# Kernel optimization log

Measured on AMD Instinct MI355X. Metric: run time of the kernel, lower is better.

The kernel has to match this reference:

```python
import jax, jax.numpy as jnp
import numpy as np

H = 8        # num_heads
DH = 64      # head_dim
DV = 64      # value_dim
DQ = 256     # query_dim
DHIT = 256   # hit_feature_dim
DMLP = 512   # query_dim * mlp_hidden_dim_multiplier
EPS = 1e-5


def _layernorm(x, g, b):
    m = jnp.mean(x, axis=-1, keepdims=True)
    v = jnp.mean(jnp.square(x - m), axis=-1, keepdims=True)
    return (x - m) * jax.lax.rsqrt(v + EPS) * g + b


def setup_inputs() -> dict:
    key = jax.random.key(0)
    ks = jax.random.split(key, 10)
    B, K, N = 8, 64, 16384
    s = 0.02
    return {
        "slot_representations": jax.random.normal(ks[0], (B, K, DQ), jnp.float32),
        "hit_features": jax.random.normal(ks[1], (B, N, DHIT), jnp.float32),
        "ln1_g": jnp.ones((DQ,), jnp.float32),
        "ln1_b": jnp.zeros((DQ,), jnp.float32),
        "Wq": jax.random.normal(ks[2], (DQ, H * DH), jnp.float32) * s,
        "Wk": jax.random.normal(ks[3], (DHIT, H * DH), jnp.float32) * s,
        "Wv": jax.random.normal(ks[4], (DHIT, H * DV), jnp.float32) * s,
        "W1": jax.random.normal(ks[5], (H * DV, DMLP), jnp.float32) * s,
        "b1": jnp.zeros((DMLP,), jnp.float32),
        "W2": jax.random.normal(ks[6], (DMLP, DQ), jnp.float32) * s,
        "b2": jnp.zeros((DQ,), jnp.float32),
        "ln2_g": jnp.ones((DQ,), jnp.float32),
        "ln2_b": jnp.zeros((DQ,), jnp.float32),
    }


def reference(slot_representations, hit_features, ln1_g, ln1_b, Wq, Wk, Wv,
              W1, b1, W2, b2, ln2_g, ln2_b):
    B, K, _ = slot_representations.shape
    _, N, _ = hit_features.shape
    scale = DH ** -0.5
    slots_norm = _layernorm(slot_representations, ln1_g, ln1_b)
    q = (slots_norm @ Wq).reshape(B, K, H, DH)          # [B,K,H,DH]
    k = (hit_features @ Wk).reshape(B, N, H, DH)        # [B,N,H,DH]
    v = (hit_features @ Wv).reshape(B, N, H, DV)        # [B,N,H,DV]
    logits = jnp.einsum('bkhd,bnhd->bhkn', q, k) * scale
    attn = jax.nn.softmax(logits, axis=-1)              # [B,H,K,N]
    att_v = jnp.einsum('bhkn,bnhd->bkhd', attn, v).reshape(B, K, H * DV)
    mlp_out = jax.nn.relu(att_v @ W1 + b1) @ W2 + b2
    return _layernorm(slot_representations + mlp_out, ln2_g, ln2_b)
```

## Files before the change

kernel.cpp:

```cpp
#include <hip/hip_runtime.h>
#include <hip/hip_bf16.h>

#define HH   8
#define Bb   8
#define Kk   64
#define Nn   16384
#define DQd  256
#define EPSf 1e-5f
#define NCH  32
#define CHK  512
#define SUB  32
#define NSUB (CHK / SUB)

typedef __bf16 bf16_t;
typedef __bf16 bf16x8 __attribute__((ext_vector_type(8)));
typedef __bf16 bf16x4 __attribute__((ext_vector_type(4)));
typedef __bf16 bf16x2 __attribute__((ext_vector_type(2)));
typedef float  f32x4  __attribute__((ext_vector_type(4)));
typedef float  f32x16 __attribute__((ext_vector_type(16)));

#define MFMA16(a, b, c) __builtin_amdgcn_mfma_f32_16x16x32_bf16((a), (b), (c), 0, 0, 0)
#define MFMA32(a, b, c) __builtin_amdgcn_mfma_f32_32x32x16_bf16((a), (b), (c), 0, 0, 0)

static __device__ __forceinline__ int pk2(float x, float y) {
    bf16x2 v; v[0] = (bf16_t)x; v[1] = (bf16_t)y;
    return __builtin_bit_cast(int, v);
}

static __device__ __forceinline__ void pack_tile(const f32x16 Sv, int hi, bf16x8* out) {
    #pragma unroll
    for (int kc = 0; kc < 2; ++kc) {
        const int oc = kc * 8;
        int Lp0 = pk2(Sv[oc + 0], Sv[oc + 1]);
        int Lp1 = pk2(Sv[oc + 2], Sv[oc + 3]);
        int Hp0 = pk2(Sv[oc + 4], Sv[oc + 5]);
        int Hp1 = pk2(Sv[oc + 6], Sv[oc + 7]);
        int Lx0 = __shfl_xor(Lp0, 32, 64);
        int Lx1 = __shfl_xor(Lp1, 32, 64);
        int Hx0 = __shfl_xor(Hp0, 32, 64);
        int Hx1 = __shfl_xor(Hp1, 32, 64);
        int4 bi;
        bi.x = hi ? Hx0 : Lp0;
        bi.y = hi ? Hx1 : Lp1;
        bi.z = hi ? Hp0 : Lx0;
        bi.w = hi ? Hp1 : Lx1;
        out[kc] = __builtin_bit_cast(bf16x8, bi);
    }
}

static __device__ __forceinline__ void store8(bf16_t* dst, float4 a, float4 b) {
    bf16x8 o;
    o[0] = (bf16_t)a.x; o[1] = (bf16_t)a.y; o[2] = (bf16_t)a.z; o[3] = (bf16_t)a.w;
    o[4] = (bf16_t)b.x; o[5] = (bf16_t)b.y; o[6] = (bf16_t)b.z; o[7] = (bf16_t)b.w;
    *(bf16x8*)dst = o;
}

__global__ __launch_bounds__(256) void k0_ln(
    const float* __restrict__ slots, const float* __restrict__ g1,
    const float* __restrict__ bb1, const float* __restrict__ Wv,
    bf16_t* __restrict__ norm, bf16_t* __restrict__ WvT)
{
    const int t = threadIdx.x;
    if (blockIdx.x >= 32) {
        const int h = blockIdx.x - 32;
        const int dv = t & 63, dq = t >> 6;
        #pragma unroll
        for (int i = 0; i < 16; ++i) {
            int d = dq * 64 + i * 4;
            bf16x4 o;
            #pragma unroll
            for (int j = 0; j < 4; ++j)
                o[j] = (bf16_t)Wv[(size_t)(d + j) * 512 + h * 64 + dv];
            *(bf16x4*)&WvT[(size_t)(h * 64 + dv) * 256 + d] = o;
        }
        return;
    }
    const int b = blockIdx.x >> 2, rg = blockIdx.x & 3;
    const int w = t >> 6, lane = t & 63;
    float4 gv = *(const float4*)&g1[lane * 4];
    float4 bv = *(const float4*)&bb1[lane * 4];
    #pragma unroll
    for (int i = 0; i < 4; ++i) {
        int row = rg * 16 + w * 4 + i;
        float4 x = *(const float4*)&slots[((size_t)b * Kk + row) * DQd + lane * 4];
        float s = x.x + x.y + x.z + x.w;
        for (int m = 1; m < 64; m <<= 1) s += __shfl_xor(s, m, 64);
        float mean = s * (1.0f / 256.0f);
        float dx = x.x - mean, dy = x.y - mean, dz = x.z - mean, dw = x.w - mean;
        float v2 = dx * dx + dy * dy + dz * dz + dw * dw;
        for (int m = 1; m < 64; m <<= 1) v2 += __shfl_xor(v2, m, 64);
        float rs = rsqrtf(v2 * (1.0f / 256.0f) + EPSf);
        bf16x4 o;
        o[0] = (bf16_t)(dx * rs * gv.x + bv.x);
        o[1] = (bf16_t)(dy * rs * gv.y + bv.y);
        o[2] = (bf16_t)(dz * rs * gv.z + bv.z);
        o[3] = (bf16_t)(dw * rs * gv.w + bv.w);
        *(bf16x4*)&norm[((size_t)b * Kk + row) * 256 + lane * 4] = o;
    }
}

__global__ __launch_bounds__(256) void k0m(
    const float* __restrict__ Wq, const float* __restrict__ Wk,
    bf16_t* __restrict__ MT)
{
    __shared__ float scr4[4][32 * 33];
    const int h = blockIdx.x >> 2, rt = blockIdx.x & 3;
    const int t = threadIdx.x;
    const int w = t >> 6, lane = t & 63, l31 = lane & 31, hi = lane >> 5;

    f32x16 acc[2][2] = {};
    for (int kc = 0; kc < 4; ++kc) {
        bf16x8 af[2], bfr[2];
        #pragma unroll
        for (int mt = 0; mt < 2; ++mt) {
            const float* src = &Wq[(size_t)(w * 64 + mt * 32 + l31) * 512 + h * 64 + kc * 16 + hi * 8];
            float4 u0 = ((const float4*)src)[0], u1 = ((const float4*)src)[1];
            af[mt][0] = (bf16_t)u0.x; af[mt][1] = (bf16_t)u0.y;
            af[mt][2] = (bf16_t)u0.z; af[mt][3] = (bf16_t)u0.w;
            af[mt][4] = (bf16_t)u1.x; af[mt][5] = (bf16_t)u1.y;
            af[mt][6] = (bf16_t)u1.z; af[mt][7] = (bf16_t)u1.w;
        }
        #pragma unroll
        for (int nt = 0; nt < 2; ++nt) {
            const float* src = &Wk[(size_t)(rt * 64 + nt * 32 + l31) * 512 + h * 64 + kc * 16 + hi * 8];
            float4 u0 = ((const float4*)src)[0], u1 = ((const float4*)src)[1];
            bfr[nt][0] = (bf16_t)u0.x; bfr[nt][1] = (bf16_t)u0.y;
            bfr[nt][2] = (bf16_t)u0.z; bfr[nt][3] = (bf16_t)u0.w;
            bfr[nt][4] = (bf16_t)u1.x; bfr[nt][5] = (bf16_t)u1.y;
            bfr[nt][6] = (bf16_t)u1.z; bfr[nt][7] = (bf16_t)u1.w;
        }
        #pragma unroll
        for (int mt = 0; mt < 2; ++mt)
            #pragma unroll
            for (int nt = 0; nt < 2; ++nt)
                acc[mt][nt] = MFMA32(af[mt], bfr[nt], acc[mt][nt]);
    }
    float* scr = scr4[w];
    #pragma unroll
    for (int mt = 0; mt < 2; ++mt)
        for (int nt = 0; nt < 2; ++nt) {
            #pragma unroll
            for (int r = 0; r < 16; ++r) {
                int m = (r & 3) + 8 * (r >> 2) + 4 * hi;
                scr[m * 33 + l31] = acc[mt][nt][r] * 0.125f;
            }
            #pragma unroll
            for (int j = 0; j < 16; ++j) {
                int c = rt * 64 + nt * 32 + hi * 16 + j;
                MT[((size_t)(h * 256 + c)) * 256 + w * 64 + mt * 32 + l31]
                    = (bf16_t)scr[l31 * 33 + hi * 16 + j];
            }
        }
}

__global__ __launch_bounds__(256) void k1n(
    const bf16_t* __restrict__ norm, const bf16_t* __restrict__ MT,
    bf16_t* __restrict__ qt)
{
    __shared__ float scr4[4][32 * 33];
    const int bid = blockIdx.x;
    const int ch = bid & 1, h = (bid >> 1) & 7, b = bid >> 4;
    const int t = threadIdx.x;
    const int w = t >> 6, lane = t & 63, l31 = lane & 31, hi = lane >> 5;
    const int colbase = ch * 128 + w * 32;

    const bf16_t* mbase = MT + ((size_t)(h * 256 + colbase + l31)) * 256 + hi * 8;
    const bf16_t* nbase = norm + ((size_t)(b * 64 + l31)) * 256 + hi * 8;

    f32x16 acc[2] = {};
    for (int kc = 0; kc < 16; ++kc) {
        bf16x8 af = *(const bf16x8*)(mbase + kc * 16);
        bf16x8 b0 = *(const bf16x8*)(nbase + kc * 16);
        bf16x8 b1 = *(const bf16x8*)(nbase + (size_t)32 * 256 + kc * 16);
        acc[0] = MFMA32(af, b0, acc[0]);
        acc[1] = MFMA32(af, b1, acc[1]);
    }
    float* scr = scr4[w];
    size_t qbase = (size_t)(b * HH + h) * 64;
    #pragma unroll
    for (int nt = 0; nt < 2; ++nt) {
        #pragma unroll
        for (int r = 0; r < 16; ++r) {
            int m = (r & 3) + 8 * (r >> 2) + 4 * hi;
            scr[m * 33 + l31] = acc[nt][r];
        }
        #pragma unroll
        for (int j = 0; j < 16; ++j) {
            qt[(qbase + nt * 32 + hi * 16 + j) * 256 + colbase + l31]
                = (bf16_t)scr[l31 * 33 + hi * 16 + j];
        }
    }
}

__global__ __launch_bounds__(512) void k3_attn(
    const float* __restrict__ hit, const bf16_t* __restrict__ qt,
    const bf16_t* __restrict__ WvT, bf16_t* __restrict__ nump,
    float* __restrict__ lp)
{
    __shared__ alignas(16) bf16_t hs[2][SUB * 256];
    __shared__ alignas(16) bf16_t vb[2][16 * 512];

    const int bid = blockIdx.x;
    const int c  = bid & 31;
    const int hg = (bid >> 5) & 1;
    const int b  = bid >> 6;
    const int t  = threadIdx.x;
    const int w = t >> 6, lane = t & 63;
    const int l31 = lane & 31, hi = lane >> 5;
    const int hl = w >> 1;
    const int qh = w & 1;
    const int h  = hg * 4 + hl;
    const int bh = b * HH + h;

    bf16x8 qf[16], wf[16];
    {
        const bf16_t* qrow = qt + ((size_t)bh * 64 + qh * 32 + l31) * 256 + hi * 8;
        const bf16_t* wrow = WvT + ((size_t)(h * 64 + qh * 32 + l31)) * 256 + hi * 8;
        #pragma unroll
        for (int ks = 0; ks < 16; ++ks) {
            qf[ks] = *(const bf16x8*)(qrow + ks * 16);
            wf[ks] = *(const bf16x8*)(wrow + ks * 16);
        }
    }

    f32x16 accO = {};
    f32x16 accX = {};
    float ls = 0.f;

    const float* hbase = hit + ((size_t)b * Nn + c * CHK) * 256;
    const int row0 = t >> 5, g0 = t & 31;
    const int sw0 = (g0 ^ (row0 & 7)) * 8;
    const int sw1 = (g0 ^ ((row0 + 16) & 7)) * 8;

    float4 pA0, pA1, pB0, pB1;
#define PREFETCH(ss) do { \
        const float* s0_ = hbase + (size_t)(ss) * SUB * 256 + (size_t)row0 * 256 + g0 * 8; \
        pA0 = ((const float4*)s0_)[0]; pA1 = ((const float4*)s0_)[1]; \
        const float* s1_ = s0_ + 16 * 256; \
        pB0 = ((const float4*)s1_)[0]; pB1 = ((const float4*)s1_)[1]; \
    } while (0)

    PREFETCH(0);
    store8(&hs[0][row0 * 256 + sw0], pA0, pA1);
    store8(&hs[0][(row0 + 16) * 256 + sw1], pB0, pB1);
    PREFETCH(1);
    __syncthreads();

    const int xr = l31 & 7;

    for (int s = 0; s < NSUB; ++s) {
        const int cur = s & 1;
        const bf16_t* hrow = &hs[cur][l31 * 256];

        f32x16 St = {}, Vt = {};
        #pragma unroll
        for (int ks = 0; ks < 16; ++ks) {
            bf16x8 A = *(const bf16x8*)(hrow + (((2 * ks + hi) ^ xr) * 8));
            Vt = MFMA32(A, wf[ks], Vt);
            St = MFMA32(A, qf[ks], St);
        }

        if (s + 1 < NSUB) {
            store8(&hs[cur ^ 1][row0 * 256 + sw0], pA0, pA1);
            store8(&hs[cur ^ 1][(row0 + 16) * 256 + sw1], pB0, pB1);
        }
        if (s + 2 < NSUB) PREFETCH(s + 2);

        #pragma unroll
        for (int r = 0; r < 16; ++r) {
            float e = __expf(St[r]);
            St[r] = e;
            ls += e;
        }
        bf16x8 Pf[2];
        pack_tile(St, hi, Pf);
        {
            bf16x8 Vf[2];
            pack_tile(Vt, hi, Vf);
            *(bf16x8*)&vb[cur][((hl * 2 + 0) * 2 + qh) * 512 + lane * 8] = Vf[0];
            *(bf16x8*)&vb[cur][((hl * 2 + 1) * 2 + qh) * 512 + lane * 8] = Vf[1];
        }
        __syncthreads();

        {
            bf16x8 vo0 = *(const bf16x8*)&vb[cur][((hl * 2 + 0) * 2 + qh) * 512 + lane * 8];
            bf16x8 vx0 = *(const bf16x8*)&vb[cur][((hl * 2 + 0) * 2 + (1 - qh)) * 512 + lane * 8];
            bf16x8 vo1 = *(const bf16x8*)&vb[cur][((hl * 2 + 1) * 2 + qh) * 512 + lane * 8];
            bf16x8 vx1 = *(const bf16x8*)&vb[cur][((hl * 2 + 1) * 2 + (1 - qh)) * 512 + lane * 8];
            accO = MFMA32(Pf[0], vo0, accO);
            accX = MFMA32(Pf[0], vx0, accX);
            accO = MFMA32(Pf[1], vo1, accO);
            accX = MFMA32(Pf[1], vx1, accX);
        }
    }
#undef PREFETCH

    {
        float lt = ls + __shfl_xor(ls, 32, 64);
        if (hi == 0)
            lp[((size_t)bh * NCH + c) * 64 + qh * 32 + l31] = lt;
    }
    {
        size_t nbase = ((size_t)bh * NCH + c) * 64 * 64;
        #pragma unroll
        for (int r = 0; r < 16; ++r) {
            int q = qh * 32 + (r & 3) + 8 * (r >> 2) + 4 * hi;
            size_t ro = nbase + (size_t)q * 64;
            nump[ro + qh * 32 + l31]       = (bf16_t)accO[r];
            nump[ro + (1 - qh) * 32 + l31] = (bf16_t)accX[r];
        }
    }
}

__global__ __launch_bounds__(256) void k35_comb(
    const bf16_t* __restrict__ nump, const float* __restrict__ lp,
    bf16_t* __restrict__ X)
{
    const int bh = blockIdx.x >> 1, qhb = blockIdx.x & 1;
    const int b = bh >> 3, h = bh & 7;
    const int t = threadIdx.x;
    const int q = qhb * 32 + (t >> 3), g = t & 7;
    float s8[8] = {};
    float lsum = 0.f;
    #pragma unroll 4
    for (int cc = 0; cc < NCH; ++cc) {
        size_t base = ((size_t)bh * NCH + cc) * 64 + q;
        bf16x8 v = *(const bf16x8*)&nump[base * 64 + g * 8];
        #pragma unroll
        for (int j = 0; j < 8; ++j) s8[j] += (float)v[j];
        lsum += lp[base];
    }
    float inv = 1.0f / lsum;
    bf16x8 o;
    #pragma unroll
    for (int j = 0; j < 8; ++j) o[j] = (bf16_t)(s8[j] * inv);
    *(bf16x8*)&X[((size_t)b * 64 + q) * 512 + h * 64 + g * 8] = o;
}

__global__ __launch_bounds__(256) void k4a_mlp1(
    const bf16_t* __restrict__ X, const float* __restrict__ W1,
    const float* __restrict__ b1, bf16_t* __restrict__ H)
{
    __shared__ float scr[32 * 33];
    const int rt = blockIdx.x >> 4, ct = blockIdx.x & 15;
    const int t = threadIdx.x;
    const int w = t >> 6, lane = t & 63, l31 = lane & 31, hi = lane >> 5;
    const int colbase = ct * 32;

    for (int i = t; i < 32 * 33; i += 256) scr[i] = 0.f;

    const bf16_t* xrow = X + ((size_t)(rt * 32 + l31)) * 512 + hi * 8;
    f32x16 acc = {};
    #pragma unroll
    for (int k8 = 0; k8 < 8; ++k8) {
        int kc = w * 8 + k8;
        bf16x8 af;
        #pragma unroll
        for (int j = 0; j < 8; ++j)
            af[j] = (bf16_t)W1[(size_t)(kc * 16 + hi * 8 + j) * 512 + colbase + l31];
        bf16x8 bfr = *(const bf16x8*)(xrow + kc * 16);
        acc = MFMA32(af, bfr, acc);
    }
    __syncthreads();
    #pragma unroll
    for (int r = 0; r < 16; ++r) {
        int m = (r & 3) + 8 * (r >> 2) + 4 * hi;
        atomicAdd(&scr[m * 33 + l31], acc[r]);
    }
    __syncthreads();
    const float bia = b1[colbase + l31];
    #pragma unroll
    for (int jj = 0; jj < 4; ++jj) {
        int j = w * 4 + jj;
        float v = scr[l31 * 33 + hi * 16 + j] + bia;
        v = fmaxf(v, 0.f);
        H[((size_t)(rt * 32 + hi * 16 + j)) * 512 + colbase + l31] = (bf16_t)v;
    }
}

__global__ __launch_bounds__(256) void k4b_gemm(
    const bf16_t* __restrict__ H, const float* __restrict__ W2,
    const float* __restrict__ b2, const float* __restrict__ slots,
    float* __restrict__ ys)
{
    __shared__ float scr[32 * 33];
    const int b = blockIdx.x >> 4, rtt = (blockIdx.x >> 3) & 1, ct = blockIdx.x & 7;
    const int t = threadIdx.x;
    const int w = t >> 6, lane = t & 63, l31 = lane & 31, hi = lane >> 5;
    const int colbase = ct * 32;
    const int rowbase = b * 64 + rtt * 32;

    for (int i = t; i < 32 * 33; i += 256) scr[i] = 0.f;

    const bf16_t* hrow = H + ((size_t)(rowbase + l31)) * 512 + hi * 8;
    f32x16 acc = {};
    #pragma unroll
    for (int k8 = 0; k8 < 8; ++k8) {
        int kc = w * 8 + k8;
        bf16x8 af;
        #pragma unroll
        for (int j = 0; j < 8; ++j)
            af[j] = (bf16_t)W2[(size_t)(kc * 16 + hi * 8 + j) * 256 + colbase + l31];
        bf16x8 bfr = *(const bf16x8*)(hrow + kc * 16);
        acc = MFMA32(af, bfr, acc);
    }
    __syncthreads();
    #pragma unroll
    for (int r = 0; r < 16; ++r) {
        int m = (r & 3) + 8 * (r >> 2) + 4 * hi;
        atomicAdd(&scr[m * 33 + l31], acc[r]);
    }
    __syncthreads();
    const float b2c = b2[colbase + l31];
    #pragma unroll
    for (int jj = 0; jj < 4; ++jj) {
        int j = w * 4 + jj;
        int row = rowbase + hi * 16 + j;
        float v = scr[l31 * 33 + hi * 16 + j] + b2c
                + slots[(size_t)row * 256 + colbase + l31];
        ys[(size_t)row * 256 + colbase + l31] = v;
    }
}

__global__ __launch_bounds__(256) void k4c_ln2(
    const float* __restrict__ ys, const float* __restrict__ g2,
    const float* __restrict__ bb2, float* __restrict__ out)
{
    const int t = threadIdx.x;
    const int w = t >> 6, lane = t & 63;
    float4 gv = *(const float4*)&g2[lane * 4];
    float4 bv = *(const float4*)&bb2[lane * 4];
    #pragma unroll
    for (int rr = 0; rr < 2; ++rr) {
        int row = blockIdx.x * 8 + w * 2 + rr;
        float4 x = *(const float4*)&ys[(size_t)row * 256 + lane * 4];
        float s = x.x + x.y + x.z + x.w;
        for (int m = 1; m < 64; m <<= 1) s += __shfl_xor(s, m, 64);
        float mean = s * (1.0f / 256.0f);
        float dx = x.x - mean, dy = x.y - mean, dz = x.z - mean, dw = x.w - mean;
        float v2 = dx * dx + dy * dy + dz * dz + dw * dw;
        for (int m = 1; m < 64; m <<= 1) v2 += __shfl_xor(v2, m, 64);
        float rs = rsqrtf(v2 * (1.0f / 256.0f) + EPSf);
        float4 o;
        o.x = dx * rs * gv.x + bv.x;
        o.y = dy * rs * gv.y + bv.y;
        o.z = dz * rs * gv.z + bv.z;
        o.w = dw * rs * gv.w + bv.w;
        *(float4*)&out[(size_t)row * 256 + lane * 4] = o;
    }
}

extern "C" void kernel_launch(void* const* d_in, const int* in_sizes, int n_in,
                              void* d_out, int out_size, void* d_ws, size_t ws_size,
                              hipStream_t stream) {
    (void)in_sizes; (void)n_in; (void)out_size; (void)ws_size;
    const float* slots = (const float*)d_in[0];
    const float* hit   = (const float*)d_in[1];
    const float* g1    = (const float*)d_in[2];
    const float* bb1   = (const float*)d_in[3];
    const float* Wq    = (const float*)d_in[4];
    const float* Wk    = (const float*)d_in[5];
    const float* Wv    = (const float*)d_in[6];
    const float* W1    = (const float*)d_in[7];
    const float* b1v   = (const float*)d_in[8];
    const float* W2    = (const float*)d_in[9];
    const float* b2v   = (const float*)d_in[10];
    const float* g2    = (const float*)d_in[11];
    const float* bb2   = (const float*)d_in[12];
    float* out = (float*)d_out;

    char* wsp = (char*)d_ws;
    bf16_t* qt   = (bf16_t*)wsp;
    float*  ys   = (float*) wsp;
    bf16_t* WvT  = (bf16_t*)(wsp + (size_t)2097152);
    bf16_t* nump = (bf16_t*)(wsp + (size_t)2359296);
    bf16_t* MT   = (bf16_t*)(wsp + (size_t)2359296);
    bf16_t* norm = (bf16_t*)(wsp + (size_t)2359296 + 1048576);
    float*  lp   = (float*) (wsp + (size_t)19136512);
    bf16_t* X    = (bf16_t*)(wsp + (size_t)19660800);
    bf16_t* H    = (bf16_t*)(wsp + (size_t)20185088);

    hipLaunchKernelGGL(k0_ln, dim3(40), dim3(256), 0, stream,
                       slots, g1, bb1, Wv, norm, WvT);
    hipLaunchKernelGGL(k0m, dim3(32), dim3(256), 0, stream,
                       Wq, Wk, MT);
    hipLaunchKernelGGL(k1n, dim3(128), dim3(256), 0, stream,
                       norm, MT, qt);
    hipLaunchKernelGGL(k3_attn, dim3(Bb * 2 * NCH), dim3(512), 0, stream,
                       hit, qt, WvT, nump, lp);
    hipLaunchKernelGGL(k35_comb, dim3(128), dim3(256), 0, stream,
                       nump, lp, X);
    hipLaunchKernelGGL(k4a_mlp1, dim3(256), dim3(256), 0, stream,
                       X, W1, b1v, H);
    hipLaunchKernelGGL(k4b_gemm, dim3(128), dim3(256), 0, stream,
                       H, W2, b2v, slots, ys);
    hipLaunchKernelGGL(k4c_ln2, dim3(64), dim3(256), 0, stream,
                       ys, g2, bb2, out);
}
```

Measured before the change: 295.5 us.

## Fuse weight-prep kernels and merge final GEMM with residual LayerNorm

Merges the two prologue kernels (LayerNorm/Wv transpose and the Wq·Wk^T product) into one launch by block-index dispatch. Fuses the W2 GEMM, bias, residual add and final LayerNorm into a single kernel that keeps the pre-norm rows in shared memory instead of writing them to workspace. This removes two kernel launches and a global round trip for the intermediate, but the fused tail runs on only 16 blocks, each doing a full K=512 reduction serially per wave with uncoalesced W2 loads. That shrinks parallelism in the tail considerably.

```diff
diff --git a/kernel.cpp b/kernel.cpp
--- a/kernel.cpp
+++ b/kernel.cpp
@@ -55,12 +55,65 @@
     *(bf16x8*)dst = o;
 }
 
-__global__ __launch_bounds__(256) void k0_ln(
+__global__ __launch_bounds__(256) void k0_all(
     const float* __restrict__ slots, const float* __restrict__ g1,
-    const float* __restrict__ bb1, const float* __restrict__ Wv,
-    bf16_t* __restrict__ norm, bf16_t* __restrict__ WvT)
+    const float* __restrict__ bb1, const float* __restrict__ Wq,
+    const float* __restrict__ Wk, const float* __restrict__ Wv,
+    bf16_t* __restrict__ norm, bf16_t* __restrict__ WvT,
+    bf16_t* __restrict__ MT)
 {
     const int t = threadIdx.x;
+    if (blockIdx.x >= 40) {
+        __shared__ float scr4[4][32 * 33];
+        const int idm = blockIdx.x - 40;
+        const int h = idm >> 2, rt = idm & 3;
+        const int w = t >> 6, lane = t & 63, l31 = lane & 31, hi = lane >> 5;
+
+        f32x16 acc[2][2] = {};
+        for (int kc = 0; kc < 4; ++kc) {
+            bf16x8 af[2], bfr[2];
+            #pragma unroll
+            for (int mt = 0; mt < 2; ++mt) {
+                const float* src = &Wq[(size_t)(w * 64 + mt * 32 + l31) * 512 + h * 64 + kc * 16 + hi * 8];
+                float4 u0 = ((const float4*)src)[0], u1 = ((const float4*)src)[1];
+                af[mt][0] = (bf16_t)u0.x; af[mt][1] = (bf16_t)u0.y;
+                af[mt][2] = (bf16_t)u0.z; af[mt][3] = (bf16_t)u0.w;
+                af[mt][4] = (bf16_t)u1.x; af[mt][5] = (bf16_t)u1.y;
+                af[mt][6] = (bf16_t)u1.z; af[mt][7] = (bf16_t)u1.w;
+            }
+            #pragma unroll
+            for (int nt = 0; nt < 2; ++nt) {
+                const float* src = &Wk[(size_t)(rt * 64 + nt * 32 + l31) * 512 + h * 64 + kc * 16 + hi * 8];
+                float4 u0 = ((const float4*)src)[0], u1 = ((const float4*)src)[1];
+                bfr[nt][0] = (bf16_t)u0.x; bfr[nt][1] = (bf16_t)u0.y;
+                bfr[nt][2] = (bf16_t)u0.z; bfr[nt][3] = (bf16_t)u0.w;
+                bfr[nt][4] = (bf16_t)u1.x; bfr[nt][5] = (bf16_t)u1.y;
+                bfr[nt][6] = (bf16_t)u1.z; bfr[nt][7] = (bf16_t)u1.w;
+            }
+            #pragma unroll
+            for (int mt = 0; mt < 2; ++mt)
+                #pragma unroll
+                for (int nt = 0; nt < 2; ++nt)
+                    acc[mt][nt] = MFMA32(af[mt], bfr[nt], acc[mt][nt]);
+        }
+        float* scr = scr4[w];
+        #pragma unroll
+        for (int mt = 0; mt < 2; ++mt)
+            for (int nt = 0; nt < 2; ++nt) {
+                #pragma unroll
+                for (int r = 0; r < 16; ++r) {
+                    int m = (r & 3) + 8 * (r >> 2) + 4 * hi;
+                    scr[m * 33 + l31] = acc[mt][nt][r] * 0.125f;
+                }
+                #pragma unroll
+                for (int j = 0; j < 16; ++j) {
+                    int c = rt * 64 + nt * 32 + hi * 16 + j;
+                    MT[((size_t)(h * 256 + c)) * 256 + w * 64 + mt * 32 + l31]
+                        = (bf16_t)scr[l31 * 33 + hi * 16 + j];
+                }
+            }
+        return;
+    }
     if (blockIdx.x >= 32) {
         const int h = blockIdx.x - 32;
         const int dv = t & 63, dq = t >> 6;
@@ -99,60 +152,6 @@
     }
 }
 
-__global__ __launch_bounds__(256) void k0m(
-    const float* __restrict__ Wq, const float* __restrict__ Wk,
-    bf16_t* __restrict__ MT)
-{
-    __shared__ float scr4[4][32 * 33];
-    const int h = blockIdx.x >> 2, rt = blockIdx.x & 3;
-    const int t = threadIdx.x;
-    const int w = t >> 6, lane = t & 63, l31 = lane & 31, hi = lane >> 5;
-
-    f32x16 acc[2][2] = {};
-    for (int kc = 0; kc < 4; ++kc) {
-        bf16x8 af[2], bfr[2];
-        #pragma unroll
-        for (int mt = 0; mt < 2; ++mt) {
-            const float* src = &Wq[(size_t)(w * 64 + mt * 32 + l31) * 512 + h * 64 + kc * 16 + hi * 8];
-            float4 u0 = ((const float4*)src)[0], u1 = ((const float4*)src)[1];
-            af[mt][0] = (bf16_t)u0.x; af[mt][1] = (bf16_t)u0.y;
-            af[mt][2] = (bf16_t)u0.z; af[mt][3] = (bf16_t)u0.w;
-            af[mt][4] = (bf16_t)u1.x; af[mt][5] = (bf16_t)u1.y;
-            af[mt][6] = (bf16_t)u1.z; af[mt][7] = (bf16_t)u1.w;
-        }
-        #pragma unroll
-        for (int nt = 0; nt < 2; ++nt) {
-            const float* src = &Wk[(size_t)(rt * 64 + nt * 32 + l31) * 512 + h * 64 + kc * 16 + hi * 8];
-            float4 u0 = ((const float4*)src)[0], u1 = ((const float4*)src)[1];
-            bfr[nt][0] = (bf16_t)u0.x; bfr[nt][1] = (bf16_t)u0.y;
-            bfr[nt][2] = (bf16_t)u0.z; bfr[nt][3] = (bf16_t)u0.w;
-            bfr[nt][4] = (bf16_t)u1.x; bfr[nt][5] = (bf16_t)u1.y;
-            bfr[nt][6] = (bf16_t)u1.z; bfr[nt][7] = (bf16_t)u1.w;
-        }
-        #pragma unroll
-        for (int mt = 0; mt < 2; ++mt)
-            #pragma unroll
-            for (int nt = 0; nt < 2; ++nt)
-                acc[mt][nt] = MFMA32(af[mt], bfr[nt], acc[mt][nt]);
-    }
-    float* scr = scr4[w];
-    #pragma unroll
-    for (int mt = 0; mt < 2; ++mt)
-        for (int nt = 0; nt < 2; ++nt) {
-            #pragma unroll
-            for (int r = 0; r < 16; ++r) {
-                int m = (r & 3) + 8 * (r >> 2) + 4 * hi;
-                scr[m * 33 + l31] = acc[mt][nt][r] * 0.125f;
-            }
-            #pragma unroll
-            for (int j = 0; j < 16; ++j) {
-                int c = rt * 64 + nt * 32 + hi * 16 + j;
-                MT[((size_t)(h * 256 + c)) * 256 + w * 64 + mt * 32 + l31]
-                    = (bf16_t)scr[l31 * 33 + hi * 16 + j];
-            }
-        }
-}
-
 __global__ __launch_bounds__(256) void k1n(
     const bf16_t* __restrict__ norm, const bf16_t* __restrict__ MT,
     bf16_t* __restrict__ qt)
@@ -378,75 +377,70 @@
     }
 }
 
-__global__ __launch_bounds__(256) void k4b_gemm(
+__global__ __launch_bounds__(256) void k4bc(
     const bf16_t* __restrict__ H, const float* __restrict__ W2,
     const float* __restrict__ b2, const float* __restrict__ slots,
-    float* __restrict__ ys)
-{
-    __shared__ float scr[32 * 33];
-    const int b = blockIdx.x >> 4, rtt = (blockIdx.x >> 3) & 1, ct = blockIdx.x & 7;
+    const float* __restrict__ g2, const float* __restrict__ bb2,
+    float* __restrict__ out)
+{
+    __shared__ float ysL[32 * 260];
+    __shared__ float scr4[4][32 * 33];
+    const int b = blockIdx.x >> 1, rhalf = blockIdx.x & 1;
+    const int rowbase = b * 64 + rhalf * 32;
     const int t = threadIdx.x;
     const int w = t >> 6, lane = t & 63, l31 = lane & 31, hi = lane >> 5;
-    const int colbase = ct * 32;
-    const int rowbase = b * 64 + rtt * 32;
-
-    for (int i = t; i < 32 * 33; i += 256) scr[i] = 0.f;
 
     const bf16_t* hrow = H + ((size_t)(rowbase + l31)) * 512 + hi * 8;
-    f32x16 acc = {};
-    #pragma unroll
-    for (int k8 = 0; k8 < 8; ++k8) {
-        int kc = w * 8 + k8;
-        bf16x8 af;
-        #pragma unroll
-        for (int j = 0; j < 8; ++j)
-            af[j] = (bf16_t)W2[(size_t)(kc * 16 + hi * 8 + j) * 256 + colbase + l31];
-        bf16x8 bfr = *(const bf16x8*)(hrow + kc * 16);
-        acc = MFMA32(af, bfr, acc);
+    float* scr = scr4[w];
+
+    #pragma unroll
+    for (int mc = 0; mc < 2; ++mc) {
+        const int colbase = w * 64 + mc * 32;
+        f32x16 acc = {};
+        for (int kc = 0; kc < 32; ++kc) {
+            bf16x8 af;
+            #pragma unroll
+            for (int j = 0; j < 8; ++j)
+                af[j] = (bf16_t)W2[(size_t)(kc * 16 + hi * 8 + j) * 256 + colbase + l31];
+            bf16x8 bfr = *(const bf16x8*)(hrow + kc * 16);
+            acc = MFMA32(af, bfr, acc);
+        }
+        const float b2c = b2[colbase + l31];
+        #pragma unroll
+        for (int r = 0; r < 16; ++r) {
+            int m = (r & 3) + 8 * (r >> 2) + 4 * hi;
+            scr[m * 33 + l31] = acc[r];
+        }
+        #pragma unroll
+        for (int j = 0; j < 16; ++j) {
+            int rl = hi * 16 + j;
+            float v = scr[l31 * 33 + rl] + b2c
+                    + slots[(size_t)(rowbase + rl) * 256 + colbase + l31];
+            ysL[rl * 260 + colbase + l31] = v;
+        }
     }
     __syncthreads();
-    #pragma unroll
-    for (int r = 0; r < 16; ++r) {
-        int m = (r & 3) + 8 * (r >> 2) + 4 * hi;
-        atomicAdd(&scr[m * 33 + l31], acc[r]);
-    }
-    __syncthreads();
-    const float b2c = b2[colbase + l31];
-    #pragma unroll
-    for (int jj = 0; jj < 4; ++jj) {
-        int j = w * 4 + jj;
-        int row = rowbase + hi * 16 + j;
-        float v = scr[l31 * 33 + hi * 16 + j] + b2c
-                + slots[(size_t)row * 256 + colbase + l31];
-        ys[(size_t)row * 256 + colbase + l31] = v;
-    }
-}
-
-__global__ __launch_bounds__(256) void k4c_ln2(
-    const float* __restrict__ ys, const float* __restrict__ g2,
-    const float* __restrict__ bb2, float* __restrict__ out)
-{
-    const int t = threadIdx.x;
-    const int w = t >> 6, lane = t & 63;
-    float4 gv = *(const float4*)&g2[lane * 4];
-    float4 bv = *(const float4*)&bb2[lane * 4];
-    #pragma unroll
-    for (int rr = 0; rr < 2; ++rr) {
-        int row = blockIdx.x * 8 + w * 2 + rr;
-        float4 x = *(const float4*)&ys[(size_t)row * 256 + lane * 4];
-        float s = x.x + x.y + x.z + x.w;
-        for (int m = 1; m < 64; m <<= 1) s += __shfl_xor(s, m, 64);
-        float mean = s * (1.0f / 256.0f);
-        float dx = x.x - mean, dy = x.y - mean, dz = x.z - mean, dw = x.w - mean;
-        float v2 = dx * dx + dy * dy + dz * dz + dw * dw;
-        for (int m = 1; m < 64; m <<= 1) v2 += __shfl_xor(v2, m, 64);
-        float rs = rsqrtf(v2 * (1.0f / 256.0f) + EPSf);
-        float4 o;
-        o.x = dx * rs * gv.x + bv.x;
-        o.y = dy * rs * gv.y + bv.y;
-        o.z = dz * rs * gv.z + bv.z;
-        o.w = dw * rs * gv.w + bv.w;
-        *(float4*)&out[(size_t)row * 256 + lane * 4] = o;
+    {
+        float4 gv = *(const float4*)&g2[lane * 4];
+        float4 bv = *(const float4*)&bb2[lane * 4];
+        #pragma unroll
+        for (int rr = 0; rr < 8; ++rr) {
+            int rl = w * 8 + rr;
+            float4 x = *(const float4*)&ysL[rl * 260 + lane * 4];
+            float s = x.x + x.y + x.z + x.w;
+            for (int m = 1; m < 64; m <<= 1) s += __shfl_xor(s, m, 64);
+            float mean = s * (1.0f / 256.0f);
+            float dx = x.x - mean, dy = x.y - mean, dz = x.z - mean, dw = x.w - mean;
+            float v2 = dx * dx + dy * dy + dz * dz + dw * dw;
+            for (int m = 1; m < 64; m <<= 1) v2 += __shfl_xor(v2, m, 64);
+            float rs = rsqrtf(v2 * (1.0f / 256.0f) + EPSf);
+            float4 o;
+            o.x = dx * rs * gv.x + bv.x;
+            o.y = dy * rs * gv.y + bv.y;
+            o.z = dz * rs * gv.z + bv.z;
+            o.w = dw * rs * gv.w + bv.w;
+            *(float4*)&out[(size_t)(rowbase + rl) * 256 + lane * 4] = o;
+        }
     }
 }
 
@@ -471,7 +465,6 @@
 
     char* wsp = (char*)d_ws;
     bf16_t* qt   = (bf16_t*)wsp;
-    float*  ys   = (float*) wsp;
     bf16_t* WvT  = (bf16_t*)(wsp + (size_t)2097152);
     bf16_t* nump = (bf16_t*)(wsp + (size_t)2359296);
     bf16_t* MT   = (bf16_t*)(wsp + (size_t)2359296);
@@ -480,10 +473,8 @@
     bf16_t* X    = (bf16_t*)(wsp + (size_t)19660800);
     bf16_t* H    = (bf16_t*)(wsp + (size_t)20185088);
 
-    hipLaunchKernelGGL(k0_ln, dim3(40), dim3(256), 0, stream,
-                       slots, g1, bb1, Wv, norm, WvT);
-    hipLaunchKernelGGL(k0m, dim3(32), dim3(256), 0, stream,
-                       Wq, Wk, MT);
+    hipLaunchKernelGGL(k0_all, dim3(72), dim3(256), 0, stream,
+                       slots, g1, bb1, Wq, Wk, Wv, norm, WvT, MT);
     hipLaunchKernelGGL(k1n, dim3(128), dim3(256), 0, stream,
                        norm, MT, qt);
     hipLaunchKernelGGL(k3_attn, dim3(Bb * 2 * NCH), dim3(512), 0, stream,
@@ -492,8 +483,6 @@
                        nump, lp, X);
     hipLaunchKernelGGL(k4a_mlp1, dim3(256), dim3(256), 0, stream,
                        X, W1, b1v, H);
-    hipLaunchKernelGGL(k4b_gemm, dim3(128), dim3(256), 0, stream,
-                       H, W2, b2v, slots, ys);
-    hipLaunchKernelGGL(k4c_ln2, dim3(64), dim3(256), 0, stream,
-                       ys, g2, bb2, out);
-}
+    hipLaunchKernelGGL(k4bc, dim3(16), dim3(256), 0, stream,
+                       H, W2, b2v, slots, g2, bb2, out);
+}
```

Result: slower. 305.5 us (+3.4%).
